# Performance work log

Measured on AMD Instinct MI355X. Metric: run time of the kernel, lower is better.

The kernel has to match this reference:

```python
import jax, jax.numpy as jnp
import numpy as np

A = 9          # num anchors (RPN.anchor_list)
H = W = 32     # feature-map spatial size (scaled-up from 7x7)
HID = 256      # ProposalModule hidden dim
THRESH = 0.5       # inference() thresh default
NMS_THRESH = 0.7   # inference() nms_thresh default
N = H * W * A


def _conv(x, w, b):
    y = jax.lax.conv_general_dilated(x, w, (1, 1), 'SAME',
                                     dimension_numbers=('NCHW', 'OIHW', 'NCHW'))
    return y + b[None, :, None, None]


def _pairwise_iou(boxes):
    # boxes: (N,4) [x1,y1,x2,y2]
    x1, y1, x2, y2 = boxes[:, 0], boxes[:, 1], boxes[:, 2], boxes[:, 3]
    area = jnp.maximum(x2 - x1, 0.) * jnp.maximum(y2 - y1, 0.)
    iw = jnp.maximum(jnp.minimum(x2[:, None], x2[None, :]) - jnp.maximum(x1[:, None], x1[None, :]), 0.)
    ih = jnp.maximum(jnp.minimum(y2[:, None], y2[None, :]) - jnp.maximum(y1[:, None], y1[None, :]), 0.)
    inter = iw * ih
    return inter / (area[:, None] + area[None, :] - inter + 1e-8)


def _nms_keep(boxes, scores, valid, iou_thresh):
    # greedy NMS over ALL boxes; invalid (below conf-thresh) boxes start suppressed
    n = boxes.shape[0]
    order = jnp.argsort(-scores)
    b = boxes[order]
    v = valid[order]
    iou = _pairwise_iou(b)            # (N,N) -- dominant memory traffic
    idx = jnp.arange(n)

    def body(i, sup):
        alive = jnp.logical_not(sup[i])
        return sup | (alive & (iou[i] > iou_thresh) & (idx > i))

    sup = jax.lax.fori_loop(0, n, body, jnp.logical_not(v))
    return jnp.zeros(n, bool).at[order].set(jnp.logical_not(sup))


def setup_inputs() -> dict:
    key = jax.random.key(0)
    ks = jax.random.split(key, 4)
    feat = jax.random.normal(ks[0], (1, 1280, H, W), jnp.float32)
    anchors_wh = jnp.array([[1, 1], [2, 2], [3, 3], [4, 4], [5, 5],
                            [2, 3], [3, 2], [3, 5], [5, 3]], jnp.float32)
    w1 = jax.random.normal(ks[1], (HID, 1280, 3, 3), jnp.float32) * 0.01
    b1 = jnp.zeros((HID,), jnp.float32)
    w2 = jax.random.normal(ks[2], (6 * A, HID, 1, 1), jnp.float32) * 0.05
    b2 = jax.random.normal(ks[3], (6 * A,), jnp.float32) * 0.05
    return {"feat": feat, "anchors_wh": anchors_wh, "w1": w1, "b1": b1, "w2": w2, "b2": b2}


def reference(feat, anchors_wh, w1, b1, w2, b2):
    # ProposalModule: 3x3 conv + LeakyReLU + 1x1 conv to 6A channels (dropout is identity at inference)
    h = jax.nn.leaky_relu(_conv(feat, w1, b1), 0.01)
    out = _conv(h, w2, b2)[0].reshape(A, 6, H, W)   # batch 1 -> (A,6,H,W)
    conf = jax.nn.sigmoid(out[:, 0])                 # (A,H,W), sigmoid(conf_scores[:,0])
    offs = out[:, 2:6].transpose(0, 2, 3, 1)         # (A,H,W,4) = offsets.permute(0,2,3,1)

    # GenerateGrid: cell centers at +0.5; GenerateAnchor: wh-sized boxes on each center
    xs = jnp.arange(W, dtype=feat.dtype) + 0.5
    ys = jnp.arange(H, dtype=feat.dtype) + 0.5
    cx = xs[None, None, :]
    cy = ys[None, :, None]
    aw = anchors_wh[:, 0][:, None, None]
    ah = anchors_wh[:, 1][:, None, None]

    tx, ty, tw, th = offs[..., 0], offs[..., 1], offs[..., 2], offs[..., 3]
    pcx = cx + tx * aw
    pcy = cy + ty * ah
    pw = aw * jnp.exp(tw)
    ph = ah * jnp.exp(th)
    boxes = jnp.stack([pcx - pw / 2, pcy - ph / 2, pcx + pw / 2, pcy + ph / 2], -1)  # (A,H,W,4)

    conf_f = conf.transpose(1, 2, 0).reshape(-1)          # (H*W*A,) = permute(1,2,0).reshape(-1)
    boxes_f = boxes.transpose(1, 2, 0, 3).reshape(-1, 4)  # (H*W*A,4)

    valid = conf_f > THRESH
    scores = jnp.where(valid, conf_f, -1.0)
    keep = _nms_keep(boxes_f, scores, valid, NMS_THRESH)

    k = keep.astype(boxes_f.dtype)[:, None]
    # fixed-shape masked output: kept rows are [x1,y1,x2,y2,conf], suppressed rows are 0
    return jnp.concatenate([boxes_f * k, conf_f[:, None] * k], axis=-1)  # (N,5)
```

## Files before the change

### kernel.cpp

```cpp
#include <hip/hip_runtime.h>
#include <math.h>

#define NPIX 1024
#define NBOX 9216
#define ECAP 6144

typedef unsigned long long u64;

#define O_PART     0u
#define O_H        0u
#define O_BOXES    1048576u
#define O_CONF     1196032u
#define O_KEYS     1232896u
#define O_ORDER    1306624u
#define O_SBOX     1343488u
#define O_SAREA    1490944u
#define O_EDGES    1527808u
#define O_KEEPW    1552384u
#define O_RPART    1553920u
#define O_VCNT     16777216u
#define O_ECNT     16777220u


__global__ __launch_bounds__(256, 4) void conv1_kernel(const float* __restrict__ feat,
                                                       const float* __restrict__ w1,
                                                       float* __restrict__ partial) {
    const int kc  = blockIdx.x;
    const int cog = blockIdx.y;
    const int tid = threadIdx.x;
    const int x0 = (tid & 7) * 4;
    const int y  = tid >> 3;
    const int ci0 = kc * 80;
    const int co0 = cog * 4;

    __shared__ float sf[8 * 34 * 32];

    for (int e = tid; e < 8 * 2 * 32; e += 256) {
        int ci_l = e >> 6, r = (e >> 5) & 1, c = e & 31;
        sf[(ci_l * 34 + r * 33) * 32 + c] = 0.f;
    }

    float acc[4][4];
#pragma unroll
    for (int a = 0; a < 4; ++a)
#pragma unroll
        for (int b = 0; b < 4; ++b) acc[a][b] = 0.f;

    const float* wbase = w1 + (size_t)co0 * 11520 + (size_t)ci0 * 9;

    for (int chunk = 0; chunk < 10; ++chunk) {
        const int cbase = ci0 + chunk * 8;
        __syncthreads();
        {
            const float4* fg = (const float4*)(feat + (size_t)cbase * NPIX);
#pragma unroll
            for (int k = 0; k < 8; ++k) {
                int e = tid + k * 256;
                int ci_l = e >> 8, rem = e & 255;
                int row = rem >> 3, f4c = rem & 7;
                float4 v = fg[ci_l * 256 + rem];
                *(float4*)&sf[(ci_l * 34 + row + 1) * 32 + f4c * 4] = v;
            }
        }
        __syncthreads();

#pragma unroll
        for (int cil = 0; cil < 8; ++cil) {
            float f[3][6];
            const float* base = &sf[(cil * 34 + y) * 32];
#pragma unroll
            for (int dy = 0; dy < 3; ++dy) {
                const float* rp = base + dy * 32;
                float4 mid = *(const float4*)(rp + x0);
                float lft = __int_as_float(__builtin_amdgcn_update_dpp(
                    0, __float_as_int(mid.w), 0x111 , 0xF, 0xF, true));
                float rgt = __int_as_float(__builtin_amdgcn_update_dpp(
                    0, __float_as_int(mid.x), 0x101 , 0xF, 0xF, true));
                f[dy][0] = (x0 == 0) ? 0.f : lft;
                f[dy][1] = mid.x; f[dy][2] = mid.y; f[dy][3] = mid.z; f[dy][4] = mid.w;
                f[dy][5] = (x0 == 28) ? 0.f : rgt;
            }
#pragma unroll
            for (int co = 0; co < 4; ++co) {
                const float* wrow = wbase + (size_t)co * 11520 +
                                    (size_t)(chunk * 8 + cil) * 9;
                float wv[9];
#pragma unroll
                for (int t = 0; t < 9; ++t) wv[t] = wrow[t];
#pragma unroll
                for (int dy = 0; dy < 3; ++dy)
#pragma unroll
                    for (int dx = 0; dx < 3; ++dx) {
                        float wgt = wv[dy * 3 + dx];
#pragma unroll
                        for (int px = 0; px < 4; ++px)
                            acc[co][px] = fmaf(f[dy][px + dx], wgt, acc[co][px]);
                    }
            }
        }
    }

    const int pix = y * 32 + x0;
#pragma unroll
    for (int co = 0; co < 4; ++co) {
        float4 v = {acc[co][0], acc[co][1], acc[co][2], acc[co][3]};
        *(float4*)&partial[((size_t)kc * 256 + co0 + co) * NPIX + pix] = v;
    }
}

__global__ __launch_bounds__(256) void conv1_reduce(float* part_h,
                                                    const float* __restrict__ b1) {
    int i = blockIdx.x * 256 + threadIdx.x;
    float s = b1[i >> 10];
#pragma unroll
    for (int kc = 0; kc < 16; ++kc) s += part_h[(size_t)kc * 262144 + i];
    part_h[i] = s > 0.f ? s : 0.01f * s;
}

__global__ __launch_bounds__(256) void conv2_decode(const float* __restrict__ h,
                                                    const float* __restrict__ w2,
                                                    const float* __restrict__ b2,
                                                    const float* __restrict__ anchors,
                                                    float* __restrict__ boxes,
                                                    float* __restrict__ conf_arr,
                                                    u64* __restrict__ keys,
                                                    int* __restrict__ Vcnt) {
    int gid = blockIdx.x * 256 + threadIdx.x;
    int box = gid >> 2, q = gid & 3;
    int a = box >> 10, p = box & 1023;
    const float* hq  = h + (size_t)(q * 64) * NPIX + p;
    const float* wb  = w2 + (size_t)(a * 6) * 256 + q * 64;
    float s0 = 0.f, s2 = 0.f, s3 = 0.f, s4 = 0.f, s5 = 0.f;
#pragma unroll 4
    for (int ci = 0; ci < 64; ++ci) {
        float hv = hq[(size_t)ci * NPIX];
        s0 = fmaf(hv, wb[0 * 256 + ci], s0);
        s2 = fmaf(hv, wb[2 * 256 + ci], s2);
        s3 = fmaf(hv, wb[3 * 256 + ci], s3);
        s4 = fmaf(hv, wb[4 * 256 + ci], s4);
        s5 = fmaf(hv, wb[5 * 256 + ci], s5);
    }
    s0 += __shfl_xor(s0, 1); s0 += __shfl_xor(s0, 2);
    s2 += __shfl_xor(s2, 1); s2 += __shfl_xor(s2, 2);
    s3 += __shfl_xor(s3, 1); s3 += __shfl_xor(s3, 2);
    s4 += __shfl_xor(s4, 1); s4 += __shfl_xor(s4, 2);
    s5 += __shfl_xor(s5, 1); s5 += __shfl_xor(s5, 2);
    if (q == 0) {
        s0 += b2[a * 6 + 0];
        s2 += b2[a * 6 + 2];
        s3 += b2[a * 6 + 3];
        s4 += b2[a * 6 + 4];
        s5 += b2[a * 6 + 5];
        float conf = 1.f / (1.f + expf(-s0));
        float x = (float)(p & 31), yy = (float)(p >> 5);
        float cx = x + 0.5f, cy = yy + 0.5f;
        float aw = anchors[a * 2 + 0], ah = anchors[a * 2 + 1];
        float pcx = cx + s2 * aw, pcy = cy + s3 * ah;
        float pw = aw * expf(s4), ph = ah * expf(s5);
        int idx = p * 9 + a;
        boxes[idx * 4 + 0] = pcx - pw / 2.f;
        boxes[idx * 4 + 1] = pcy - ph / 2.f;
        boxes[idx * 4 + 2] = pcx + pw / 2.f;
        boxes[idx * 4 + 3] = pcy + ph / 2.f;
        conf_arr[idx] = conf;
        bool valid = conf > 0.5f;
        float score = valid ? conf : -1.0f;
        unsigned int sb = __float_as_uint(score);
        sb = (sb & 0x80000000u) ? ~sb : (sb | 0x80000000u);
        keys[idx] = ((u64)sb << 32) | (unsigned int)(~idx);
        if (valid) atomicAdd(Vcnt, 1);
    }
}

__global__ __launch_bounds__(256) void rank_partial(const u64* __restrict__ keys,
                                                    int* __restrict__ rpart) {
    __shared__ u64 sk[256];
    int i = blockIdx.x * 256 + threadIdx.x;
    sk[threadIdx.x] = keys[blockIdx.y * 256 + threadIdx.x];
    __syncthreads();
    u64 ki = keys[i];
    int c = 0;
#pragma unroll 8
    for (int j = 0; j < 256; ++j) c += (sk[j] > ki) ? 1 : 0;
    rpart[blockIdx.y * NBOX + i] = c;
}

__global__ __launch_bounds__(256) void rank_reduce_gather(const int* __restrict__ rpart,
                                                          const float* __restrict__ boxes,
                                                          int* __restrict__ order,
                                                          float* __restrict__ sbox,
                                                          float* __restrict__ sarea) {
    int i = blockIdx.x * 256 + threadIdx.x;
    int r = 0;
    for (int b = 0; b < 36; ++b) r += rpart[b * NBOX + i];
    order[r] = i;
    float x1 = boxes[i * 4 + 0], y1 = boxes[i * 4 + 1];
    float x2 = boxes[i * 4 + 2], y2 = boxes[i * 4 + 3];
    sbox[r * 4 + 0] = x1; sbox[r * 4 + 1] = y1;
    sbox[r * 4 + 2] = x2; sbox[r * 4 + 3] = y2;
    sarea[r] = fmaxf(x2 - x1, 0.f) * fmaxf(y2 - y1, 0.f);
}

__global__ __launch_bounds__(256) void nms_edges(const float* __restrict__ sbox,
                                                 const float* __restrict__ sarea,
                                                 const int* __restrict__ Vp,
                                                 unsigned* __restrict__ edges,
                                                 int* __restrict__ Ecnt) {
    int i = blockIdx.x;
    int V = *Vp;
    if (i >= V) return;
    float x1i = sbox[i * 4 + 0], y1i = sbox[i * 4 + 1];
    float x2i = sbox[i * 4 + 2], y2i = sbox[i * 4 + 3];
    float ai = sarea[i];
    int lane = threadIdx.x & 63;
    for (int j = i + 1 + threadIdx.x; ; j += 256) {
        bool active = (j < V);
        if (__ballot(active) == 0ull) break;
        bool hit = false;
        if (active) {
            float x1j = sbox[j * 4 + 0], y1j = sbox[j * 4 + 1];
            float x2j = sbox[j * 4 + 2], y2j = sbox[j * 4 + 3];
            float iw = fmaxf(fminf(x2i, x2j) - fmaxf(x1i, x1j), 0.f);
            float ih = fmaxf(fminf(y2i, y2j) - fmaxf(y1i, y1j), 0.f);
            float inter = iw * ih;
            float iou = inter / (ai + sarea[j] - inter + 1e-8f);
            hit = iou > 0.7f;
        }
        u64 bal = __ballot(hit);
        if (bal) {
            int cnt = __popcll(bal);
            unsigned base = 0;
            if (lane == 0) base = (unsigned)atomicAdd(Ecnt, cnt);
            base = (unsigned)__shfl((int)base, 0, 64);
            if (hit) {
                int pos = (int)base + __popcll(bal & ((1ull << lane) - 1ull));
                if (pos < ECAP) edges[pos] = ((unsigned)j << 16) | (unsigned)i;
            }
        }
    }
}

__global__ __launch_bounds__(256) void nms_resolve(const unsigned* __restrict__ edges,
                                                   const int* __restrict__ Ep,
                                                   const int* __restrict__ Vp,
                                                   u64* __restrict__ keepw) {
    __shared__ unsigned se[ECAP];
    __shared__ unsigned ss[ECAP];
    __shared__ u64 sup[144];
    const int tid = threadIdx.x;
    int E = *Ep; if (E > ECAP) E = ECAP;
    const int V = *Vp;
    for (int e = tid; e < E; e += 256) se[e] = edges[e];
    for (int w = tid; w < 144; w += 256) sup[w] = 0;
    __syncthreads();
    for (int e = tid; e < E; e += 256) {
        unsigned k = se[e];
        int r = 0;
        for (int q = 0; q < E; ++q) r += (se[q] < k) ? 1 : 0;
        ss[r] = k;
    }
    __syncthreads();
    if (tid == 0) {
        for (int e = 0; e < E; ++e) {
            unsigned k = ss[e];
            int i = (int)(k & 0xffffu), j = (int)(k >> 16);
            if (!((sup[i >> 6] >> (i & 63)) & 1ull))
                sup[j >> 6] |= 1ull << (j & 63);
        }
    }
    __syncthreads();
    for (int w = tid; w < 144; w += 256) {
        int base = w * 64;
        u64 vm;
        if (base + 64 <= V) vm = ~0ull;
        else if (base >= V) vm = 0ull;
        else vm = (1ull << (V - base)) - 1ull;
        keepw[w] = ~sup[w] & vm;
    }
}

__global__ __launch_bounds__(256) void finalize(const int* __restrict__ order,
                                                const int* __restrict__ Vp,
                                                const u64* __restrict__ keepw,
                                                const float* __restrict__ boxes,
                                                const float* __restrict__ conf_arr,
                                                float* __restrict__ out) {
    int p = blockIdx.x * 256 + threadIdx.x;
    int V = *Vp;
    int o = order[p];
    bool keep = false;
    if (p < V) keep = (keepw[p >> 6] >> (p & 63)) & 1ull;
    float k = keep ? 1.f : 0.f;
    out[o * 5 + 0] = boxes[o * 4 + 0] * k;
    out[o * 5 + 1] = boxes[o * 4 + 1] * k;
    out[o * 5 + 2] = boxes[o * 4 + 2] * k;
    out[o * 5 + 3] = boxes[o * 4 + 3] * k;
    out[o * 5 + 4] = conf_arr[o] * k;
}

extern "C" void kernel_launch(void* const* d_in, const int* in_sizes, int n_in,
                              void* d_out, int out_size, void* d_ws, size_t ws_size,
                              hipStream_t stream) {
    const float* feat    = (const float*)d_in[0];
    const float* anchors = (const float*)d_in[1];
    const float* w1      = (const float*)d_in[2];
    const float* b1      = (const float*)d_in[3];
    const float* w2      = (const float*)d_in[4];
    const float* b2      = (const float*)d_in[5];
    float* out = (float*)d_out;

    char* ws = (char*)d_ws;
    float* partial = (float*)(ws + O_PART);
    float* h       = (float*)(ws + O_H);
    float* boxes   = (float*)(ws + O_BOXES);
    float* conf    = (float*)(ws + O_CONF);
    u64*   keys    = (u64*)(ws + O_KEYS);
    int* rpart     = (int*)(ws + O_RPART);
    int* order     = (int*)(ws + O_ORDER);
    float* sbox    = (float*)(ws + O_SBOX);
    float* sarea   = (float*)(ws + O_SAREA);
    int* Vcnt      = (int*)(ws + O_VCNT);
    int* Ecnt      = (int*)(ws + O_ECNT);
    u64* keepw     = (u64*)(ws + O_KEEPW);
    unsigned* edges = (unsigned*)(ws + O_EDGES);

    hipMemsetAsync(Vcnt, 0, 8, stream);

    conv1_kernel<<<dim3(16, 64), 256, 0, stream>>>(feat, w1, partial);
    conv1_reduce<<<1024, 256, 0, stream>>>(partial, b1);
    conv2_decode<<<144, 256, 0, stream>>>(h, w2, b2, anchors, boxes, conf, keys, Vcnt);
    rank_partial<<<dim3(36, 36), 256, 0, stream>>>(keys, rpart);
    rank_reduce_gather<<<36, 256, 0, stream>>>(rpart, boxes, order, sbox, sarea);
    nms_edges<<<NBOX, 256, 0, stream>>>(sbox, sarea, Vcnt, edges, Ecnt);
    nms_resolve<<<1, 256, 0, stream>>>(edges, Ecnt, Vcnt, keepw);
    finalize<<<36, 256, 0, stream>>>(order, Vcnt, keepw, boxes, conf, out);
}
```

Baseline: 226.4 us.

## Fold counter reset into conv1, split conv2 reduction wider, grid-stride NMS edges

The hipMemsetAsync that zeroed the valid and edge counters is removed, and the first conv1 block now writes the zeros, which drops one stream operation. conv2_decode splits each box's 256-channel dot product over 8 lanes instead of 4 and launches twice as many blocks, adding one shuffle step per sum. nms_edges moves from one block per box (9216 blocks) to 2048 blocks that stride over the valid boxes, so fewer blocks launch only to exit early. The cost is less balanced work per block in the NMS pass, and the counter reset now depends on conv1 running before the counters are read.

New measurement: 226.1 us. Within noise of the previous version (-0.2%).

```diff
diff --git a/kernel.cpp b/kernel.cpp
--- a/kernel.cpp
+++ b/kernel.cpp
@@ -24,7 +24,8 @@
 
 __global__ __launch_bounds__(256, 4) void conv1_kernel(const float* __restrict__ feat,
                                                        const float* __restrict__ w1,
-                                                       float* __restrict__ partial) {
+                                                       float* __restrict__ partial,
+                                                       int* __restrict__ VE) {
     const int kc  = blockIdx.x;
     const int cog = blockIdx.y;
     const int tid = threadIdx.x;
@@ -32,6 +33,8 @@
     const int y  = tid >> 3;
     const int ci0 = kc * 80;
     const int co0 = cog * 4;
+
+    if (kc == 0 && cog == 0 && tid < 2) VE[tid] = 0;
 
     __shared__ float sf[8 * 34 * 32];
 
@@ -126,25 +129,25 @@
                                                     u64* __restrict__ keys,
                                                     int* __restrict__ Vcnt) {
     int gid = blockIdx.x * 256 + threadIdx.x;
-    int box = gid >> 2, q = gid & 3;
+    int box = gid >> 3, q = gid & 7;
     int a = box >> 10, p = box & 1023;
-    const float* hq  = h + (size_t)(q * 64) * NPIX + p;
-    const float* wb  = w2 + (size_t)(a * 6) * 256 + q * 64;
+    const float* hq  = h + (size_t)(q * 32) * NPIX + p;
+    const float* wq  = w2 + (size_t)(a * 6) * 256 + q * 32;
     float s0 = 0.f, s2 = 0.f, s3 = 0.f, s4 = 0.f, s5 = 0.f;
 #pragma unroll 4
-    for (int ci = 0; ci < 64; ++ci) {
+    for (int ci = 0; ci < 32; ++ci) {
         float hv = hq[(size_t)ci * NPIX];
-        s0 = fmaf(hv, wb[0 * 256 + ci], s0);
-        s2 = fmaf(hv, wb[2 * 256 + ci], s2);
-        s3 = fmaf(hv, wb[3 * 256 + ci], s3);
-        s4 = fmaf(hv, wb[4 * 256 + ci], s4);
-        s5 = fmaf(hv, wb[5 * 256 + ci], s5);
-    }
-    s0 += __shfl_xor(s0, 1); s0 += __shfl_xor(s0, 2);
-    s2 += __shfl_xor(s2, 1); s2 += __shfl_xor(s2, 2);
-    s3 += __shfl_xor(s3, 1); s3 += __shfl_xor(s3, 2);
-    s4 += __shfl_xor(s4, 1); s4 += __shfl_xor(s4, 2);
-    s5 += __shfl_xor(s5, 1); s5 += __shfl_xor(s5, 2);
+        s0 = fmaf(hv, wq[0 * 256 + ci], s0);
+        s2 = fmaf(hv, wq[2 * 256 + ci], s2);
+        s3 = fmaf(hv, wq[3 * 256 + ci], s3);
+        s4 = fmaf(hv, wq[4 * 256 + ci], s4);
+        s5 = fmaf(hv, wq[5 * 256 + ci], s5);
+    }
+    s0 += __shfl_xor(s0, 1); s0 += __shfl_xor(s0, 2); s0 += __shfl_xor(s0, 4);
+    s2 += __shfl_xor(s2, 1); s2 += __shfl_xor(s2, 2); s2 += __shfl_xor(s2, 4);
+    s3 += __shfl_xor(s3, 1); s3 += __shfl_xor(s3, 2); s3 += __shfl_xor(s3, 4);
+    s4 += __shfl_xor(s4, 1); s4 += __shfl_xor(s4, 2); s4 += __shfl_xor(s4, 4);
+    s5 += __shfl_xor(s5, 1); s5 += __shfl_xor(s5, 2); s5 += __shfl_xor(s5, 4);
     if (q == 0) {
         s0 += b2[a * 6 + 0];
         s2 += b2[a * 6 + 2];
@@ -206,35 +209,35 @@
                                                  const int* __restrict__ Vp,
                                                  unsigned* __restrict__ edges,
                                                  int* __restrict__ Ecnt) {
-    int i = blockIdx.x;
     int V = *Vp;
-    if (i >= V) return;
-    float x1i = sbox[i * 4 + 0], y1i = sbox[i * 4 + 1];
-    float x2i = sbox[i * 4 + 2], y2i = sbox[i * 4 + 3];
-    float ai = sarea[i];
     int lane = threadIdx.x & 63;
-    for (int j = i + 1 + threadIdx.x; ; j += 256) {
-        bool active = (j < V);
-        if (__ballot(active) == 0ull) break;
-        bool hit = false;
-        if (active) {
-            float x1j = sbox[j * 4 + 0], y1j = sbox[j * 4 + 1];
-            float x2j = sbox[j * 4 + 2], y2j = sbox[j * 4 + 3];
-            float iw = fmaxf(fminf(x2i, x2j) - fmaxf(x1i, x1j), 0.f);
-            float ih = fmaxf(fminf(y2i, y2j) - fmaxf(y1i, y1j), 0.f);
-            float inter = iw * ih;
-            float iou = inter / (ai + sarea[j] - inter + 1e-8f);
-            hit = iou > 0.7f;
-        }
-        u64 bal = __ballot(hit);
-        if (bal) {
-            int cnt = __popcll(bal);
-            unsigned base = 0;
-            if (lane == 0) base = (unsigned)atomicAdd(Ecnt, cnt);
-            base = (unsigned)__shfl((int)base, 0, 64);
-            if (hit) {
-                int pos = (int)base + __popcll(bal & ((1ull << lane) - 1ull));
-                if (pos < ECAP) edges[pos] = ((unsigned)j << 16) | (unsigned)i;
+    for (int i = blockIdx.x; i < V; i += 2048) {
+        float x1i = sbox[i * 4 + 0], y1i = sbox[i * 4 + 1];
+        float x2i = sbox[i * 4 + 2], y2i = sbox[i * 4 + 3];
+        float ai = sarea[i];
+        for (int j = i + 1 + threadIdx.x; ; j += 256) {
+            bool active = (j < V);
+            if (__ballot(active) == 0ull) break;
+            bool hit = false;
+            if (active) {
+                float x1j = sbox[j * 4 + 0], y1j = sbox[j * 4 + 1];
+                float x2j = sbox[j * 4 + 2], y2j = sbox[j * 4 + 3];
+                float iw = fmaxf(fminf(x2i, x2j) - fmaxf(x1i, x1j), 0.f);
+                float ih = fmaxf(fminf(y2i, y2j) - fmaxf(y1i, y1j), 0.f);
+                float inter = iw * ih;
+                float iou = inter / (ai + sarea[j] - inter + 1e-8f);
+                hit = iou > 0.7f;
+            }
+            u64 bal = __ballot(hit);
+            if (bal) {
+                int cnt = __popcll(bal);
+                unsigned base = 0;
+                if (lane == 0) base = (unsigned)atomicAdd(Ecnt, cnt);
+                base = (unsigned)__shfl((int)base, 0, 64);
+                if (hit) {
+                    int pos = (int)base + __popcll(bal & ((1ull << lane) - 1ull));
+                    if (pos < ECAP) edges[pos] = ((unsigned)j << 16) | (unsigned)i;
+                }
             }
         }
     }
@@ -324,14 +327,12 @@
     u64* keepw     = (u64*)(ws + O_KEEPW);
     unsigned* edges = (unsigned*)(ws + O_EDGES);
 
-    hipMemsetAsync(Vcnt, 0, 8, stream);
-
-    conv1_kernel<<<dim3(16, 64), 256, 0, stream>>>(feat, w1, partial);
+    conv1_kernel<<<dim3(16, 64), 256, 0, stream>>>(feat, w1, partial, Vcnt);
     conv1_reduce<<<1024, 256, 0, stream>>>(partial, b1);
-    conv2_decode<<<144, 256, 0, stream>>>(h, w2, b2, anchors, boxes, conf, keys, Vcnt);
+    conv2_decode<<<288, 256, 0, stream>>>(h, w2, b2, anchors, boxes, conf, keys, Vcnt);
     rank_partial<<<dim3(36, 36), 256, 0, stream>>>(keys, rpart);
     rank_reduce_gather<<<36, 256, 0, stream>>>(rpart, boxes, order, sbox, sarea);
-    nms_edges<<<NBOX, 256, 0, stream>>>(sbox, sarea, Vcnt, edges, Ecnt);
+    nms_edges<<<2048, 256, 0, stream>>>(sbox, sarea, Vcnt, edges, Ecnt);
     nms_resolve<<<1, 256, 0, stream>>>(edges, Ecnt, Vcnt, keepw);
     finalize<<<36, 256, 0, stream>>>(order, Vcnt, keepw, boxes, conf, out);
 }
```
